# Optimization experiments

Hardware: AMD Instinct MI355X
Metric: run time of the kernel (lower is better)

## Reference

```python
import jax, jax.numpy as jnp
import numpy as np

B, S, E, H = 4, 2048, 512, 8
D = E // H  # projection_dim per head


def setup_inputs() -> dict:
    key = jax.random.key(0)
    ks = jax.random.split(key, 5)
    scale = 1.0 / np.sqrt(E)
    return {
        "x": jax.random.normal(ks[0], (B, S, E), dtype=jnp.float32),
        "Wq": jax.random.normal(ks[1], (E, E), dtype=jnp.float32) * scale,
        "bq": jnp.zeros((E,), dtype=jnp.float32),
        "Wk": jax.random.normal(ks[2], (E, E), dtype=jnp.float32) * scale,
        "bk": jnp.zeros((E,), dtype=jnp.float32),
        "Wv": jax.random.normal(ks[3], (E, E), dtype=jnp.float32) * scale,
        "bv": jnp.zeros((E,), dtype=jnp.float32),
        "Wo": jax.random.normal(ks[4], (E, E), dtype=jnp.float32) * scale,
        "bo": jnp.zeros((E,), dtype=jnp.float32),
    }


def _split_heads(t):
    # [B,S,E] -> [B,H,S,D]
    b, s, _ = t.shape
    return t.reshape(b, s, H, D).transpose(0, 2, 1, 3)


def reference(x, Wq, bq, Wk, bk, Wv, bv, Wo, bo):
    q = _split_heads(x @ Wq + bq)  # [B,H,S,D]
    k = _split_heads(x @ Wk + bk)
    v = _split_heads(x @ Wv + bv)
    # materialized QK^T scores as in source: matmul -> scale -> softmax -> matmul
    score = jnp.einsum("bhqd,bhkd->bhqk", q, k) / jnp.sqrt(
        jnp.asarray(D, dtype=q.dtype)
    )
    weights = jax.nn.softmax(score, axis=-1)
    attn = jnp.einsum("bhqk,bhkd->bhqd", weights, v)  # [B,H,S,D]
    merged = attn.transpose(0, 2, 1, 3).reshape(x.shape[0], x.shape[1], E)
    return merged @ Wo + bo
```

## Files before the change

kernel.cpp:

```cpp
#include <hip/hip_runtime.h>
#include <hip/hip_bf16.h>
#include <stdint.h>

typedef __bf16 bf16;
typedef __bf16 bf16x2 __attribute__((ext_vector_type(2)));
typedef __bf16 bf16x4 __attribute__((ext_vector_type(4)));
typedef __bf16 bf16x8 __attribute__((ext_vector_type(8)));
typedef float f32x4 __attribute__((ext_vector_type(4)));
typedef float f32x16 __attribute__((ext_vector_type(16)));
typedef unsigned int u32x4 __attribute__((ext_vector_type(4)));

#define AS1 __attribute__((address_space(1)))
#define AS3 __attribute__((address_space(3)))


__global__ void cast_x_kernel(const float* __restrict__ x, bf16* __restrict__ xb) {
  int i = blockIdx.x * blockDim.x + threadIdx.x;
  float4 v = reinterpret_cast<const float4*>(x)[i];
  bf16x4 o = { (bf16)v.x, (bf16)v.y, (bf16)v.z, (bf16)v.w };
  *reinterpret_cast<bf16x4*>(xb + (size_t)i * 4) = o;
}

__global__ void transpose_w4_kernel(const float* __restrict__ W0, const float* __restrict__ W1,
                                    const float* __restrict__ W2, const float* __restrict__ W3,
                                    bf16* __restrict__ Wt) {
  __shared__ bf16 t[64][65];
  const float* W = blockIdx.z == 0 ? W0 : blockIdx.z == 1 ? W1 : blockIdx.z == 2 ? W2 : W3;
  bf16* dst = Wt + (size_t)blockIdx.z * 262144;
  const int c = threadIdx.x & 63, r0 = threadIdx.x >> 6;
  const int bn = blockIdx.x * 64, bk = blockIdx.y * 64;
#pragma unroll
  for (int i = 0; i < 16; ++i) {
    int r = r0 * 16 + i;
    t[c][r] = (bf16)W[(size_t)(bk + r) * 512 + bn + c];
  }
  __syncthreads();
#pragma unroll
  for (int i = 0; i < 16; ++i) {
    int n = r0 * 16 + i;
    dst[(size_t)(bn + n) * 512 + bk + c] = t[n][c];
  }
}

template<int BN, int MODE>
__global__ __launch_bounds__(256, 4) void gemm64_kernel(
    const bf16* __restrict__ A, const bf16* __restrict__ Bt,
    const float* __restrict__ bq, const float* __restrict__ bk,
    const float* __restrict__ bv, bf16* __restrict__ out_bf,
    float* __restrict__ out_f, float qscale)
{
  constexpr int NT = BN / 32;
  __shared__ bf16 As[64 * 64];
  __shared__ bf16 Bs[BN * 64];
  const int tid = threadIdx.x, lane = tid & 63, w = tid >> 6;
  const int wm = w >> 1, wn = w & 1;
  const int m0 = blockIdx.x * 64, n0g = blockIdx.y * BN;
  const int cl = lane & 15, hi = lane >> 4;
  const int lr = lane >> 3;
  const int cofs = ((lane & 7) << 4) ^ (lr << 4);

  f32x4 acc[2][NT] = {};

  for (int kt = 0; kt < 512; kt += 64) {
    __syncthreads();
#pragma unroll
    for (int c = 0; c < 2; ++c) {
      int rA = m0 + w * 16 + c * 8 + lr;
      const void* srcA = (const char*)A + ((size_t)rA * 512 + kt) * 2 + cofs;
      void* dstA = (char*)As + w * 2048 + c * 1024;
      __builtin_amdgcn_global_load_lds((const AS1 void*)srcA, (AS3 void*)dstA, 16, 0, 0);
    }
#pragma unroll
    for (int c = 0; c < NT; ++c) {
      int rB = n0g + w * (BN / 4) + c * 8 + lr;
      const void* srcB = (const char*)Bt + ((size_t)rB * 512 + kt) * 2 + cofs;
      void* dstB = (char*)Bs + w * (BN / 4) * 128 + c * 1024;
      __builtin_amdgcn_global_load_lds((const AS1 void*)srcB, (AS3 void*)dstB, 16, 0, 0);
    }
    __syncthreads();
#pragma unroll
    for (int ks = 0; ks < 2; ++ks) {
      bf16x8 af[2], bfv[NT];
#pragma unroll
      for (int mt = 0; mt < 2; ++mt) {
        int r = wm * 32 + mt * 16 + cl;
        int cb = (ks * 64 + (hi << 4)) ^ ((r & 7) << 4);
        af[mt] = *(const bf16x8*)((const char*)As + r * 128 + cb);
      }
#pragma unroll
      for (int nt = 0; nt < NT; ++nt) {
        int r = wn * (BN / 2) + nt * 16 + cl;
        int cb = (ks * 64 + (hi << 4)) ^ ((r & 7) << 4);
        bfv[nt] = *(const bf16x8*)((const char*)Bs + r * 128 + cb);
      }
#pragma unroll
      for (int mt = 0; mt < 2; ++mt)
#pragma unroll
        for (int nt = 0; nt < NT; ++nt)
          acc[mt][nt] = __builtin_amdgcn_mfma_f32_16x16x32_bf16(af[mt], bfv[nt], acc[mt][nt], 0, 0, 0);
    }
  }

  if (MODE == 0) {
    const int which = n0g >> 9;
    const float* bias = which == 0 ? bq : (which == 1 ? bk : bv);
    const float scale = which == 0 ? qscale : 1.0f;
    bf16* outb = out_bf + (size_t)which * 4194304;
    const int ncol0 = n0g & 511;
#pragma unroll
    for (int mt = 0; mt < 2; ++mt) {
#pragma unroll
      for (int nt = 0; nt < NT; ++nt) {
        int row0 = m0 + wm * 32 + mt * 16 + hi * 4;
        int col = ncol0 + wn * (BN / 2) + nt * 16 + cl;
        float bvl = bias[col];
        int h = col >> 6, d = col & 63;
#pragma unroll
        for (int i = 0; i < 4; ++i) {
          float vv = (acc[mt][nt][i] + bvl) * scale;
          int row = row0 + i;
          int b = row >> 11, s = row & 2047;
          outb[(((size_t)(b * 8 + h)) * 2048 + s) * 64 + d] = (bf16)vv;
        }
      }
    }
  } else {
#pragma unroll
    for (int mt = 0; mt < 2; ++mt) {
#pragma unroll
      for (int nt = 0; nt < NT; ++nt) {
        int row0 = m0 + wm * 32 + mt * 16 + hi * 4;
        int col = n0g + wn * (BN / 2) + nt * 16 + cl;
        float bvl = bq[col];
#pragma unroll
        for (int i = 0; i < 4; ++i)
          out_f[(size_t)(row0 + i) * 512 + col] = acc[mt][nt][i] + bvl;
      }
    }
  }
}

__global__ __launch_bounds__(512, 4) void attn_kernel(
    const bf16* __restrict__ q, const bf16* __restrict__ k,
    const bf16* __restrict__ v, bf16* __restrict__ merged)
{
  __shared__ union SU {
    struct { bf16 K[2][2][4096]; bf16 V[2][2][4096]; } s;
    struct {
      float EPf[4][64][33];
      float Msh[8][32];
      float Lsh[8][32];
      bf16  EP[4][2304];
    } e;
  } u;
  __shared__ bf16 VT[2][4096];

  const int tid = threadIdx.x, lane = tid & 63, w = tid >> 6;
  const int wl = w & 3, half = w >> 2;
  const int ht = tid & 255;
  const int l31 = lane & 31, H = lane >> 5;
  const int bh = blockIdx.x, qb = blockIdx.y;
  const int b = bh >> 3, h = bh & 7;
  const int kv0 = half << 10;

  const bf16* Q  = q + (size_t)bh * 2048 * 64;
  const bf16* Kp = k + (size_t)bh * 2048 * 64;
  const bf16* Vp = v + (size_t)bh * 2048 * 64;

  const int q0 = qb * 128 + wl * 32;
  const int kp = ht & 31;
  const int dblk = (ht >> 5) * 8;

  const int lr8 = lane >> 3;
  const int lc = lane & 7;

#define STAGE_KV(BUF, KEYBASE)                                                            \
  {                                                                                       \
    _Pragma("unroll")                                                                     \
    for (int i = 0; i < 2; ++i) {                                                         \
      int row = wl * 16 + i * 8 + lr8;                                                    \
      const void* sK = (const char*)Kp + ((size_t)((KEYBASE) + row)) * 128 + ((lc ^ lr8) << 4); \
      void* dK = (char*)u.s.K[half][BUF] + wl * 2048 + i * 1024;                          \
      __builtin_amdgcn_global_load_lds((const AS1 void*)sK, (AS3 void*)dK, 16, 0, 0);     \
      const void* sV = (const char*)Vp + ((size_t)((KEYBASE) + row)) * 128 + ((lc ^ ((row >> 1) & 7)) << 4); \
      void* dV = (char*)u.s.V[half][BUF] + wl * 2048 + i * 1024;                          \
      __builtin_amdgcn_global_load_lds((const AS1 void*)sV, (AS3 void*)dV, 16, 0, 0);     \
    }                                                                                     \
  }

  bf16x8 qf[4];
#pragma unroll
  for (int s = 0; s < 4; ++s)
    qf[s] = *(const bf16x8*)(Q + (size_t)(q0 + l31) * 64 + s * 16 + H * 8);

  f32x16 oacc[2] = {};
  float m_run = -1e30f, l_run = 0.f;

  STAGE_KV(0, kv0);
  __syncthreads();

  int cur = 0;
  for (int kt0 = kv0; kt0 < kv0 + 1024; kt0 += 64) {
    {
      const char* vb = (const char*)u.s.V[half][cur];
      const int vofs = (((ht >> 5) ^ (kp & 7)) << 4);
      bf16x8 vs0 = *(const bf16x8*)(vb + (2 * kp) * 128 + vofs);
      bf16x8 vs1 = *(const bf16x8*)(vb + (2 * kp + 1) * 128 + vofs);
#pragma unroll
      for (int j = 0; j < 8; ++j) {
        int d = dblk + j;
        bf16x2 t = { vs0[j], vs1[j] };
        *(bf16x2*)((char*)&VT[half][0] + d * 128 + ((4 * kp) ^ ((d & 7) << 4))) = t;
      }
    }
    __syncthreads();

    if (kt0 + 64 < kv0 + 1024) STAGE_KV(cur ^ 1, kt0 + 64);

    const char* kb = (const char*)u.s.K[half][cur];

#pragma unroll
    for (int ct = 0; ct < 2; ++ct) {
      f32x16 sc = {};
      {
        const int krow = ct * 32 + l31;
        bf16x8 kf[4];
#pragma unroll
        for (int s = 0; s < 4; ++s)
          kf[s] = *(const bf16x8*)(kb + krow * 128 + ((s * 32 + H * 16) ^ ((l31 & 7) << 4)));
#pragma unroll
        for (int s = 0; s < 4; ++s)
          sc = __builtin_amdgcn_mfma_f32_32x32x16_bf16(kf[s], qf[s], sc, 0, 0, 0);
      }

      float mx[8];
#pragma unroll
      for (int r = 0; r < 8; ++r) mx[r] = fmaxf(sc[r], sc[r + 8]);
      float pmax = fmaxf(fmaxf(fmaxf(mx[0], mx[1]), fmaxf(mx[2], mx[3])),
                         fmaxf(fmaxf(mx[4], mx[5]), fmaxf(mx[6], mx[7])));
      pmax = fmaxf(pmax, __shfl_xor(pmax, 32));
      if (__any(pmax > m_run + 8.f)) {
        float mn = fmaxf(m_run, pmax);
        float alpha = exp2f(m_run - mn);
        m_run = mn;
        l_run *= alpha;
#pragma unroll
        for (int dt = 0; dt < 2; ++dt)
#pragma unroll
          for (int r = 0; r < 16; ++r) oacc[dt][r] *= alpha;
      }
#pragma unroll
      for (int r = 0; r < 16; ++r) sc[r] = exp2f(sc[r] - m_run);

      float sm[8];
#pragma unroll
      for (int r = 0; r < 8; ++r) sm[r] = sc[r] + sc[r + 8];
      float rs = ((sm[0] + sm[1]) + (sm[2] + sm[3])) + ((sm[4] + sm[5]) + (sm[6] + sm[7]));
      rs += __shfl_xor(rs, 32);
      l_run += rs;

#pragma unroll
      for (int hf = 0; hf < 2; ++hf) {
        const int ks = ct * 2 + hf;
        const int g0 = 8 * hf;
        bf16x2 pa0 = { (bf16)sc[g0 + 0], (bf16)sc[g0 + 1] };
        bf16x2 pa1 = { (bf16)sc[g0 + 2], (bf16)sc[g0 + 3] };
        bf16x2 pb0 = { (bf16)sc[g0 + 4], (bf16)sc[g0 + 5] };
        bf16x2 pb1 = { (bf16)sc[g0 + 6], (bf16)sc[g0 + 7] };
        unsigned a0 = __builtin_bit_cast(unsigned, pa0);
        unsigned a1 = __builtin_bit_cast(unsigned, pa1);
        unsigned b0 = __builtin_bit_cast(unsigned, pb0);
        unsigned b1 = __builtin_bit_cast(unsigned, pb1);
        unsigned oa0 = (unsigned)__shfl_xor((int)a0, 32);
        unsigned oa1 = (unsigned)__shfl_xor((int)a1, 32);
        unsigned ob0 = (unsigned)__shfl_xor((int)b0, 32);
        unsigned ob1 = (unsigned)__shfl_xor((int)b1, 32);
        u32x4 pw = { H ? ob0 : a0, H ? ob1 : a1, H ? b0 : oa0, H ? b1 : oa1 };
        bf16x8 pf = __builtin_bit_cast(bf16x8, pw);
#pragma unroll
        for (int dt = 0; dt < 2; ++dt) {
          int d = dt * 32 + l31;
          bf16x8 vf = *(const bf16x8*)((const char*)&VT[half][0] + d * 128 + ((ks * 32 + H * 16) ^ ((d & 7) << 4)));
          oacc[dt] = __builtin_amdgcn_mfma_f32_32x32x16_bf16(vf, pf, oacc[dt], 0, 0, 0);
        }
      }
    }

    __syncthreads();
    cur ^= 1;
  }

  if (H == 0) { u.e.Msh[w][l31] = m_run; u.e.Lsh[w][l31] = l_run; }
  __syncthreads();
  const int pw = w ^ 4;
  float m_o = u.e.Msh[pw][l31], l_o = u.e.Lsh[pw][l31];
  float Mt = fmaxf(m_run, m_o);
  float denom = exp2f(m_run - Mt) * l_run + exp2f(m_o - Mt) * l_o;
  float scale = exp2f(m_run - Mt) / denom;
  if (w < 4) {
    float* ep = &u.e.EPf[wl][lane][0];
#pragma unroll
    for (int dt = 0; dt < 2; ++dt)
#pragma unroll
      for (int r = 0; r < 16; ++r) ep[dt * 16 + r] = oacc[dt][r] * scale;
  }
  __syncthreads();
  if (w >= 4) {
    const float* ep = &u.e.EPf[wl][lane][0];
#pragma unroll
    for (int dt = 0; dt < 2; ++dt)
#pragma unroll
      for (int r = 0; r < 16; ++r) {
        float val = ep[dt * 16 + r] + oacc[dt][r] * scale;
        int d = dt * 32 + (r & 3) + 8 * (r >> 2) + 4 * H;
        u.e.EP[wl][l31 * 72 + d] = (bf16)val;
      }
    __builtin_amdgcn_s_waitcnt(0);
#pragma unroll
    for (int g = 0; g < 4; ++g) {
      int qr = g * 8 + (lane >> 3);
      bf16x8 row = *(const bf16x8*)&u.e.EP[wl][qr * 72 + (lane & 7) * 8];
      *(bf16x8*)(merged + (size_t)(b * 2048 + q0 + qr) * 512 + h * 64 + (lane & 7) * 8) = row;
    }
  }
#undef STAGE_KV
}

extern "C" void kernel_launch(void* const* d_in, const int* in_sizes, int n_in,
                              void* d_out, int out_size, void* d_ws, size_t ws_size,
                              hipStream_t stream) {
  const float* x  = (const float*)d_in[0];
  const float* Wq = (const float*)d_in[1];
  const float* bq = (const float*)d_in[2];
  const float* Wk = (const float*)d_in[3];
  const float* bk = (const float*)d_in[4];
  const float* Wv = (const float*)d_in[5];
  const float* bv = (const float*)d_in[6];
  const float* Wo = (const float*)d_in[7];
  const float* bo = (const float*)d_in[8];
  float* out = (float*)d_out;

  char* ws = (char*)d_ws;
  bf16* xb  = (bf16*)(ws);
  bf16* wt  = (bf16*)(ws + 8388608);
  bf16* qkv = (bf16*)(ws + 10485760);
  bf16* mg  = (bf16*)(ws + 35651584);

  cast_x_kernel<<<4096, 256, 0, stream>>>(x, xb);
  transpose_w4_kernel<<<dim3(8, 8, 4), 256, 0, stream>>>(Wq, Wk, Wv, Wo, wt);

  const float qscale = 0.125f * 1.44269504088896f;
  gemm64_kernel<128, 0><<<dim3(128, 12), 256, 0, stream>>>(
      xb, wt, bq, bk, bv, qkv, nullptr, qscale);

  bf16* qs = qkv;
  bf16* kk = qkv + 4194304;
  bf16* vv = qkv + 8388608;

  attn_kernel<<<dim3(32, 16), 512, 0, stream>>>(qs, kk, vv, mg);

  gemm64_kernel<64, 1><<<dim3(128, 8), 256, 0, stream>>>(
      mg, wt + 786432, bo, nullptr, nullptr, nullptr, out, 1.0f);
}
```

Measured before the change: 114.4 us.

## Merge cast and weight-transpose kernels; use permlane32_swap for P fragment exchange

```diff
diff --git a/kernel.cpp b/kernel.cpp
--- a/kernel.cpp
+++ b/kernel.cpp
@@ -9,36 +9,40 @@
 typedef float f32x4 __attribute__((ext_vector_type(4)));
 typedef float f32x16 __attribute__((ext_vector_type(16)));
 typedef unsigned int u32x4 __attribute__((ext_vector_type(4)));
+typedef int i32x2 __attribute__((ext_vector_type(2)));
 
 #define AS1 __attribute__((address_space(1)))
 #define AS3 __attribute__((address_space(3)))
 
 
-__global__ void cast_x_kernel(const float* __restrict__ x, bf16* __restrict__ xb) {
-  int i = blockIdx.x * blockDim.x + threadIdx.x;
-  float4 v = reinterpret_cast<const float4*>(x)[i];
-  bf16x4 o = { (bf16)v.x, (bf16)v.y, (bf16)v.z, (bf16)v.w };
-  *reinterpret_cast<bf16x4*>(xb + (size_t)i * 4) = o;
-}
-
-__global__ void transpose_w4_kernel(const float* __restrict__ W0, const float* __restrict__ W1,
-                                    const float* __restrict__ W2, const float* __restrict__ W3,
-                                    bf16* __restrict__ Wt) {
+__global__ void prep_kernel(const float* __restrict__ x,
+                            const float* __restrict__ W0, const float* __restrict__ W1,
+                            const float* __restrict__ W2, const float* __restrict__ W3,
+                            bf16* __restrict__ xb, bf16* __restrict__ Wt) {
   __shared__ bf16 t[64][65];
-  const float* W = blockIdx.z == 0 ? W0 : blockIdx.z == 1 ? W1 : blockIdx.z == 2 ? W2 : W3;
-  bf16* dst = Wt + (size_t)blockIdx.z * 262144;
-  const int c = threadIdx.x & 63, r0 = threadIdx.x >> 6;
-  const int bn = blockIdx.x * 64, bk = blockIdx.y * 64;
-#pragma unroll
-  for (int i = 0; i < 16; ++i) {
-    int r = r0 * 16 + i;
-    t[c][r] = (bf16)W[(size_t)(bk + r) * 512 + bn + c];
-  }
-  __syncthreads();
-#pragma unroll
-  for (int i = 0; i < 16; ++i) {
-    int n = r0 * 16 + i;
-    dst[(size_t)(bn + n) * 512 + bk + c] = t[n][c];
+  const int z = blockIdx.z;
+  if (z < 4) {
+    const float* W = z == 0 ? W0 : z == 1 ? W1 : z == 2 ? W2 : W3;
+    bf16* dst = Wt + (size_t)z * 262144;
+    const int c = threadIdx.x & 63, r0 = threadIdx.x >> 6;
+    const int bn = blockIdx.x * 64, bk = blockIdx.y * 64;
+#pragma unroll
+    for (int i = 0; i < 16; ++i) {
+      int r = r0 * 16 + i;
+      t[c][r] = (bf16)W[(size_t)(bk + r) * 512 + bn + c];
+    }
+    __syncthreads();
+#pragma unroll
+    for (int i = 0; i < 16; ++i) {
+      int n = r0 * 16 + i;
+      dst[(size_t)(bn + n) * 512 + bk + c] = t[n][c];
+    }
+  } else {
+    int bi = (z - 4) * 64 + blockIdx.y * 8 + blockIdx.x;
+    int i = bi * 256 + threadIdx.x;
+    float4 v = reinterpret_cast<const float4*>(x)[i];
+    bf16x4 o = { (bf16)v.x, (bf16)v.y, (bf16)v.z, (bf16)v.w };
+    *reinterpret_cast<bf16x4*>(xb + (size_t)i * 4) = o;
   }
 }
 
@@ -271,11 +275,20 @@
         unsigned a1 = __builtin_bit_cast(unsigned, pa1);
         unsigned b0 = __builtin_bit_cast(unsigned, pb0);
         unsigned b1 = __builtin_bit_cast(unsigned, pb1);
+        u32x4 pw;
+#if __has_builtin(__builtin_amdgcn_permlane32_swap)
+        i32x2 r0 = __builtin_amdgcn_permlane32_swap((int)a0, (int)b0, false, false);
+        i32x2 r1 = __builtin_amdgcn_permlane32_swap((int)a1, (int)b1, false, false);
+        pw[0] = (unsigned)r0[0]; pw[1] = (unsigned)r1[0];
+        pw[2] = (unsigned)r0[1]; pw[3] = (unsigned)r1[1];
+#else
         unsigned oa0 = (unsigned)__shfl_xor((int)a0, 32);
         unsigned oa1 = (unsigned)__shfl_xor((int)a1, 32);
         unsigned ob0 = (unsigned)__shfl_xor((int)b0, 32);
         unsigned ob1 = (unsigned)__shfl_xor((int)b1, 32);
-        u32x4 pw = { H ? ob0 : a0, H ? ob1 : a1, H ? b0 : oa0, H ? b1 : oa1 };
+        pw[0] = H ? ob0 : a0; pw[1] = H ? ob1 : a1;
+        pw[2] = H ? b0 : oa0; pw[3] = H ? b1 : oa1;
+#endif
         bf16x8 pf = __builtin_bit_cast(bf16x8, pw);
 #pragma unroll
         for (int dt = 0; dt < 2; ++dt) {
@@ -292,8 +305,8 @@
 
   if (H == 0) { u.e.Msh[w][l31] = m_run; u.e.Lsh[w][l31] = l_run; }
   __syncthreads();
-  const int pw = w ^ 4;
-  float m_o = u.e.Msh[pw][l31], l_o = u.e.Lsh[pw][l31];
+  const int pw2 = w ^ 4;
+  float m_o = u.e.Msh[pw2][l31], l_o = u.e.Lsh[pw2][l31];
   float Mt = fmaxf(m_run, m_o);
   float denom = exp2f(m_run - Mt) * l_run + exp2f(m_o - Mt) * l_o;
   float scale = exp2f(m_run - Mt) / denom;
@@ -346,8 +359,7 @@
   bf16* qkv = (bf16*)(ws + 10485760);
   bf16* mg  = (bf16*)(ws + 35651584);
 
-  cast_x_kernel<<<4096, 256, 0, stream>>>(x, xb);
-  transpose_w4_kernel<<<dim3(8, 8, 4), 256, 0, stream>>>(Wq, Wk, Wv, Wo, wt);
+  prep_kernel<<<dim3(8, 8, 68), 256, 0, stream>>>(x, Wq, Wk, Wv, Wo, xb, wt);
 
   const float qscale = 0.125f * 1.44269504088896f;
   gemm64_kernel<128, 0><<<dim3(128, 12), 256, 0, stream>>>(
```

After: 106.7 us. 1.07x faster.
